# Performance work log

Hardware: AMD Instinct MI355X
Metric: run time of the kernel (lower is better)

The kernel has to match this reference:

```python
import jax, jax.numpy as jnp
import numpy as np
import math

B, S = 4, 1024
D_MODEL = 512
N_HEADS = 8
D_HEAD = D_MODEL // N_HEADS
D_FF = 2048
D_K_NEIGHBOR = 512.0
EPS_NORM = 1e-5
GN_EPS = 1e-5
LAMBDA_INIT = 0.8 - 0.6 * math.exp(-0.3 * 0.0)  # layer_idx = 0 -> 0.2


def _rmsnorm(x, w, eps=EPS_NORM):
    return x * jax.lax.rsqrt(jnp.mean(x * x, axis=-1, keepdims=True) + eps) * w


def _group_norm(x, gamma, beta):
    # x: [B, S, D]; torch GroupNorm(n_heads, d_model) applied on [B, D, S]:
    # normalize each (batch, group) over (d_head * S) elements, per-channel affine.
    b, s, d = x.shape
    xg = x.transpose(0, 2, 1).reshape(b, N_HEADS, D_HEAD, s)
    mean = xg.mean(axis=(2, 3), keepdims=True)
    var = ((xg - mean) ** 2).mean(axis=(2, 3), keepdims=True)
    xn = ((xg - mean) * jax.lax.rsqrt(var + GN_EPS)).reshape(b, d, s)
    xn = xn * gamma[None, :, None] + beta[None, :, None]
    return xn.transpose(0, 2, 1)


def setup_inputs() -> dict:
    key = jax.random.key(0)
    ks = jax.random.split(key, 20)
    sd = 1.0 / math.sqrt(D_MODEL)
    sdf = 1.0 / math.sqrt(D_FF)
    f32 = jnp.float32
    return {
        'x': jax.random.normal(ks[0], (B, S, D_MODEL), f32),
        'src_padding_mask': jax.random.randint(ks[1], (B, S), 0, 2).astype(jnp.int32),
        'learned_lambda': jnp.asarray(LAMBDA_INIT, f32),
        'wq_w': (jax.random.normal(ks[2], (D_MODEL, 2 * D_MODEL), f32) * sd),
        'wq_b': jnp.zeros((2 * D_MODEL,), f32),
        'wk_w': (jax.random.normal(ks[3], (D_MODEL, 2 * D_MODEL), f32) * sd),
        'wk_b': jnp.zeros((2 * D_MODEL,), f32),
        'wv_w': (jax.random.normal(ks[4], (D_MODEL, D_MODEL), f32) * sd),
        'wv_b': jnp.zeros((D_MODEL,), f32),
        'out_w': (jax.random.normal(ks[5], (D_MODEL, D_MODEL), f32) * sd),
        'out_b': jnp.zeros((D_MODEL,), f32),
        'gn_gamma': jnp.ones((D_MODEL,), f32),
        'gn_beta': jnp.zeros((D_MODEL,), f32),
        'aq_w': (jax.random.normal(ks[6], (D_MODEL, D_MODEL), f32) * sd),
        'aq_b': jnp.zeros((D_MODEL,), f32),
        'ak_w': (jax.random.normal(ks[7], (D_MODEL, D_MODEL), f32) * sd),
        'ak_b': jnp.zeros((D_MODEL,), f32),
        'wg_w': (jax.random.normal(ks[8], (D_MODEL, D_FF), f32) * sd),
        'w1_w': (jax.random.normal(ks[9], (D_MODEL, D_FF), f32) * sd),
        'w2_w': (jax.random.normal(ks[10], (D_FF, D_MODEL), f32) * sdf),
        'norm1_w': jnp.ones((D_MODEL,), f32),
        'norm2_w': jnp.ones((D_MODEL,), f32),
    }


def reference(x, src_padding_mask, learned_lambda,
              wq_w, wq_b, wk_w, wk_b, wv_w, wv_b, out_w, out_b,
              gn_gamma, gn_beta, aq_w, aq_b, ak_w, ak_b,
              wg_w, w1_w, w2_w, norm1_w, norm2_w):
    b, s, d = x.shape
    x_norm = _rmsnorm(x, norm1_w)

    # ---- neighbor affinity (layer_idx = 0 -> a = a_hat) ----
    Q = x_norm @ aq_w + aq_b
    K = x_norm @ ak_w + ak_b
    s_fwd = jnp.sum(Q[:, :-1] * K[:, 1:], axis=-1) / D_K_NEIGHBOR   # [B, S-1]
    s_bwd = jnp.sum(Q[:, 1:] * K[:, :-1], axis=-1) / D_K_NEIGHBOR
    a = 0.5 * (jax.nn.sigmoid(s_fwd) + jax.nn.sigmoid(s_bwd))        # [B, S-1]

    # ---- hierarchical mask: C[i,j] = prod(a[i:j]) = exp(L[j]-L[i]), symmetric ----
    # L is non-increasing (a in (0,1)), so prod(a[i:j]) = exp(-|L[i]-L[j]|); diag = 1.
    L = jnp.concatenate([jnp.zeros((b, 1), x.dtype), jnp.cumsum(jnp.log(a), axis=1)], axis=1)  # [B, S]
    C = jnp.exp(-jnp.abs(L[:, :, None] - L[:, None, :]))[:, None]   # [B,1,S,S]

    # ---- differential multi-head attention ----
    qp = x_norm @ wq_w + wq_b   # [B,S,2D]
    kp = x_norm @ wk_w + wk_b
    heads = lambda t: t.reshape(b, s, N_HEADS, D_HEAD).transpose(0, 2, 1, 3)
    q1, q2 = heads(qp[..., :D_MODEL]), heads(qp[..., D_MODEL:])
    k1, k2 = heads(kp[..., :D_MODEL]), heads(kp[..., D_MODEL:])
    v = heads(x_norm @ wv_w + wv_b)
    scale = 1.0 / math.sqrt(D_HEAD)
    sc1 = jnp.einsum('bhqd,bhkd->bhqk', q1, k1) * scale
    sc2 = jnp.einsum('bhqd,bhkd->bhqk', q2, k2) * scale
    pad = (src_padding_mask == 0)[:, None, None, :]
    sc1 = jnp.where(pad, -1e9, sc1)
    sc2 = jnp.where(pad, -1e9, sc2)
    aw1 = jax.nn.softmax(sc1, axis=-1)
    aw2 = jax.nn.softmax(sc2, axis=-1)
    comb = C * (aw1 - learned_lambda * aw2)
    ctx = jnp.einsum('bhqk,bhkd->bhqd', comb, v)
    ctx = ctx.transpose(0, 2, 1, 3).reshape(b, s, D_MODEL)
    ctx = _group_norm(ctx, gn_gamma, gn_beta) * (1.0 - LAMBDA_INIT)
    attn_out = ctx @ out_w + out_b

    # ---- residual + SwiGLU FFN (dropout = identity in eval) ----
    h = x + attn_out
    hn = _rmsnorm(h, norm2_w)
    ffn = (jax.nn.silu(hn @ wg_w) * (hn @ w1_w)) @ w2_w
    return h + ffn
```

## Files before the change

kernel.cpp:

```cpp
#include <hip/hip_runtime.h>
#include <math.h>

#define Bn 4
#define Sn 1024
#define DM 512
#define NH 8
#define DFF 2048
#define QKVN 2560

typedef __attribute__((ext_vector_type(8))) __bf16 bf16x8;
typedef __attribute__((ext_vector_type(2))) __bf16 bf16x2;
typedef __attribute__((ext_vector_type(4))) float f32x4;

#define MB (1u<<20)

__device__ __forceinline__ void gl_lds16(const void* g, void* l) {
    __builtin_amdgcn_global_load_lds(
        (const __attribute__((address_space(1))) void*)g,
        (__attribute__((address_space(3))) void*)l, 16, 0, 0);
}

struct TransBatch { const float* src[4]; __bf16* dst[4]; };

__global__ __launch_bounds__(256)
void transpose_kernel(TransBatch tb, int K, int N) {
    const float* w = tb.src[blockIdx.z];
    __bf16* wT = tb.dst[blockIdx.z];
    __shared__ float tile[32][33];
    int n0 = blockIdx.x * 32, k0 = blockIdx.y * 32;
    int tx = threadIdx.x, ty = threadIdx.y;
#pragma unroll
    for (int i = 0; i < 4; ++i)
        tile[ty + 8 * i][tx] = w[(size_t)(k0 + ty + 8 * i) * N + n0 + tx];
    __syncthreads();
#pragma unroll
    for (int i = 0; i < 4; ++i)
        wT[(size_t)(n0 + ty + 8 * i) * K + k0 + tx] = (__bf16)tile[tx][ty + 8 * i];
}

__global__ __launch_bounds__(256)
void pack_biases(const float* aq_b, const float* ak_b, const float* wq_b,
                 const float* wk_b, const float* wv_b,
                 float* aqk_b, float* qkv_b) {
    int t = blockIdx.x * 256 + threadIdx.x;
    if (t < 512) aqk_b[t] = aq_b[t];
    else if (t < 1024) aqk_b[t] = ak_b[t - 512];
    else if (t < 2048) qkv_b[t - 1024] = wq_b[t - 1024];
    else if (t < 3072) qkv_b[1024 + t - 2048] = wk_b[t - 2048];
    else if (t < 3584) qkv_b[2048 + t - 3072] = wv_b[t - 3072];
}

__global__ __launch_bounds__(256)
void rmsnorm_kernel(const float* __restrict__ x, const float* __restrict__ w,
                    __bf16* __restrict__ out) {
    int row = blockIdx.x;
    const float* xr = x + (size_t)row * DM;
    int t = threadIdx.x;
    float2 v = *(const float2*)&xr[2 * t];
    float ss = v.x * v.x + v.y * v.y;
#pragma unroll
    for (int off = 32; off; off >>= 1) ss += __shfl_xor(ss, off);
    __shared__ float red[4];
    int wid = t >> 6;
    if ((t & 63) == 0) red[wid] = ss;
    __syncthreads();
    float tot = red[0] + red[1] + red[2] + red[3];
    float rinv = rsqrtf(tot / (float)DM + 1e-5f);
    bf16x2 o;
    o[0] = (__bf16)(v.x * rinv * w[2 * t]);
    o[1] = (__bf16)(v.y * rinv * w[2 * t + 1]);
    *(bf16x2*)&out[(size_t)row * DM + 2 * t] = o;
}

template<int BM, int EPI>
__global__ __launch_bounds__(256)
void gemm_bf16(const __bf16* __restrict__ A, const __bf16* __restrict__ BT,
               const float* __restrict__ bias, const float* __restrict__ res,
               void* __restrict__ out, int M, int N, int K) {
    __shared__ __align__(16) char AsB[BM * 64];
    __shared__ __align__(16) char BsB[128 * 64];
    const int t = threadIdx.x;
    const int w = t >> 6, l = t & 63, c = l & 15, g = l >> 4;
    const int wr = w >> 1, wc = w & 1;
    const int bm = blockIdx.y * BM, bn = blockIdx.x * 128;
    constexpr int HM = BM / 2, WM = BM / 32;
    f32x4 acc[WM][4];
#pragma unroll
    for (int m = 0; m < WM; ++m)
#pragma unroll
        for (int n = 0; n < 4; ++n) acc[m][n] = (f32x4){0.f, 0.f, 0.f, 0.f};
    const int srow = t >> 2;
    const int kcol = ((t & 3) ^ ((t >> 3) & 3)) << 3;
    const __bf16* Ap = A + (size_t)(bm + srow) * K + kcol;
    const __bf16* Bp = BT + (size_t)(bn + srow) * K + kcol;
    char* dA = AsB + t * 16;
    char* dB = BsB + t * 16;
    char* dB2 = BsB + 4096 + t * 16;
    const int sw = (g ^ ((c >> 1) & 3)) << 4;
    for (int k0 = 0; k0 < K; k0 += 32) {
        gl_lds16(Ap + k0, dA);
        if constexpr (BM == 128) gl_lds16(Ap + (size_t)64 * K + k0, AsB + 4096 + t * 16);
        gl_lds16(Bp + k0, dB);
        gl_lds16(Bp + (size_t)64 * K + k0, dB2);
        __syncthreads();
        bf16x8 af[WM], bf_[4];
#pragma unroll
        for (int m = 0; m < WM; ++m)
            af[m] = *(const bf16x8*)(AsB + (wr * HM + m * 16 + c) * 64 + sw);
#pragma unroll
        for (int n = 0; n < 4; ++n)
            bf_[n] = *(const bf16x8*)(BsB + (wc * 64 + n * 16 + c) * 64 + sw);
#pragma unroll
        for (int m = 0; m < WM; ++m)
#pragma unroll
            for (int n = 0; n < 4; ++n)
                acc[m][n] = __builtin_amdgcn_mfma_f32_16x16x32_bf16(af[m], bf_[n], acc[m][n], 0, 0, 0);
        __syncthreads();
    }
#pragma unroll
    for (int m = 0; m < WM; ++m)
#pragma unroll
        for (int n = 0; n < 4; ++n) {
            int rowb = bm + wr * HM + m * 16 + 4 * g;
            int col = bn + wc * 64 + n * 16 + c;
            float bv = bias ? bias[col] : 0.f;
#pragma unroll
            for (int r = 0; r < 4; ++r) {
                size_t idx = (size_t)(rowb + r) * N + col;
                float val = acc[m][n][r] + bv;
                if constexpr (EPI == 0) {
                    ((__bf16*)out)[idx] = (__bf16)val;
                } else {
                    if (res) val += res[idx];
                    ((float*)out)[idx] = val;
                }
            }
        }
}

__global__ __launch_bounds__(256)
void gemm_swiglu(const __bf16* __restrict__ A, const __bf16* __restrict__ GT,
                 const __bf16* __restrict__ UT, __bf16* __restrict__ out,
                 int M, int N, int K) {
    __shared__ __align__(16) char AsB[128 * 64];
    __shared__ __align__(16) char GsB[128 * 64];
    __shared__ __align__(16) char UsB[128 * 64];
    const int t = threadIdx.x;
    const int w = t >> 6, l = t & 63, c = l & 15, g = l >> 4;
    const int wr = w >> 1, wc = w & 1;
    const int bm = blockIdx.y * 128, bn = blockIdx.x * 128;
    f32x4 accg[4][4], accu[4][4];
#pragma unroll
    for (int m = 0; m < 4; ++m)
#pragma unroll
        for (int n = 0; n < 4; ++n) {
            accg[m][n] = (f32x4){0.f, 0.f, 0.f, 0.f};
            accu[m][n] = (f32x4){0.f, 0.f, 0.f, 0.f};
        }
    const int srow = t >> 2;
    const int kcol = ((t & 3) ^ ((t >> 3) & 3)) << 3;
    const __bf16* Ap = A + (size_t)(bm + srow) * K + kcol;
    const __bf16* Gp = GT + (size_t)(bn + srow) * K + kcol;
    const __bf16* Up = UT + (size_t)(bn + srow) * K + kcol;
    const int sw = (g ^ ((c >> 1) & 3)) << 4;
    for (int k0 = 0; k0 < K; k0 += 32) {
        gl_lds16(Ap + k0, AsB + t * 16);
        gl_lds16(Ap + (size_t)64 * K + k0, AsB + 4096 + t * 16);
        gl_lds16(Gp + k0, GsB + t * 16);
        gl_lds16(Gp + (size_t)64 * K + k0, GsB + 4096 + t * 16);
        gl_lds16(Up + k0, UsB + t * 16);
        gl_lds16(Up + (size_t)64 * K + k0, UsB + 4096 + t * 16);
        __syncthreads();
        bf16x8 af[4], gf[4], uf[4];
#pragma unroll
        for (int m = 0; m < 4; ++m)
            af[m] = *(const bf16x8*)(AsB + (wr * 64 + m * 16 + c) * 64 + sw);
#pragma unroll
        for (int n = 0; n < 4; ++n) {
            gf[n] = *(const bf16x8*)(GsB + (wc * 64 + n * 16 + c) * 64 + sw);
            uf[n] = *(const bf16x8*)(UsB + (wc * 64 + n * 16 + c) * 64 + sw);
        }
#pragma unroll
        for (int m = 0; m < 4; ++m)
#pragma unroll
            for (int n = 0; n < 4; ++n) {
                accg[m][n] = __builtin_amdgcn_mfma_f32_16x16x32_bf16(af[m], gf[n], accg[m][n], 0, 0, 0);
                accu[m][n] = __builtin_amdgcn_mfma_f32_16x16x32_bf16(af[m], uf[n], accu[m][n], 0, 0, 0);
            }
        __syncthreads();
    }
#pragma unroll
    for (int m = 0; m < 4; ++m)
#pragma unroll
        for (int n = 0; n < 4; ++n) {
            int rowb = bm + wr * 64 + m * 16 + 4 * g;
            int col = bn + wc * 64 + n * 16 + c;
#pragma unroll
            for (int r = 0; r < 4; ++r) {
                float gv = accg[m][n][r];
                float uv = accu[m][n][r];
                float sg = gv / (1.f + __expf(-gv));
                out[(size_t)(rowb + r) * N + col] = (__bf16)(sg * uv);
            }
        }
}

__global__ __launch_bounds__(256)
void affinity_dots(const __bf16* __restrict__ aqk, float* __restrict__ la) {
    int i = blockIdx.x * 256 + threadIdx.x;
    int b = blockIdx.y;
    if (i >= Sn - 1) { la[b * Sn + i] = 0.f; return; }
    const __bf16* Qi = aqk + (size_t)(b * Sn + i) * 1024;
    const __bf16* Ki = Qi + 512;
    float sf = 0.f, sb = 0.f;
#pragma unroll 4
    for (int d = 0; d < DM / 8; ++d) {
        bf16x8 q0 = *(const bf16x8*)(Qi + d * 8);
        bf16x8 q1 = *(const bf16x8*)(Qi + 1024 + d * 8);
        bf16x8 k0 = *(const bf16x8*)(Ki + d * 8);
        bf16x8 k1 = *(const bf16x8*)(Ki + 1024 + d * 8);
#pragma unroll
        for (int j = 0; j < 8; ++j) {
            sf += (float)q0[j] * (float)k1[j];
            sb += (float)q1[j] * (float)k0[j];
        }
    }
    sf *= (1.f / 512.f);
    sb *= (1.f / 512.f);
    float a = 0.5f * (1.f / (1.f + __expf(-sf)) + 1.f / (1.f + __expf(-sb)));
    la[b * Sn + i] = __logf(a);
}

__global__ __launch_bounds__(256)
void scan_kernel(const float* __restrict__ la, float* __restrict__ L) {
    int b = blockIdx.x, j = threadIdx.x;
    __shared__ float sc[256];
    float4 v = *(const float4*)&la[b * Sn + 4 * j];
    float s0 = v.x, s1 = s0 + v.y, s2 = s1 + v.z, s3 = s2 + v.w;
    sc[j] = s3;
    __syncthreads();
    for (int off = 1; off < 256; off <<= 1) {
        float add = (j >= off) ? sc[j - off] : 0.f;
        __syncthreads();
        sc[j] += add;
        __syncthreads();
    }
    float base = sc[j] - s3;
    if (j == 0) L[b * Sn] = 0.f;
    L[b * Sn + 4 * j + 1] = base + s0;
    L[b * Sn + 4 * j + 2] = base + s1;
    L[b * Sn + 4 * j + 3] = base + s2;
    if (4 * j + 4 < Sn) L[b * Sn + 4 * j + 4] = base + s3;
}

__global__ __launch_bounds__(256)
void attn_mfma(const __bf16* __restrict__ qkv, const float* __restrict__ L,
               const int* __restrict__ mask, const float* __restrict__ lam_p,
               float* __restrict__ ctx) {
    int x = blockIdx.x;
    int xcd = x & 7, idx = x >> 3;
    int bh = xcd * 4 + (idx >> 4);
    int qb = idx & 15;
    int b = bh >> 3, h = bh & 7;
    const int t = threadIdx.x;
    const int w = t >> 6, l = t & 63, c = l & 15, g = l >> 4;

    __shared__ __align__(16) char KldsB[64 * 256];
    __shared__ __align__(16) char VtB[64 * 128];
    __shared__ __align__(16) char PldsB[2][64 * 128];
    __shared__ float Lk_s[64];
    __shared__ float msk_s[64];
    __shared__ float fs_s[2][64];
    __shared__ float ls_s[2][64];

    const int q0 = qb * 64;
    const int qg = q0 + 16 * w + c;
    float Lq = L[b * Sn + qg];
    float lam = lam_p[0];
    bf16x8 qf[2][2];
#pragma unroll
    for (int mat = 0; mat < 2; ++mat)
#pragma unroll
        for (int dh = 0; dh < 2; ++dh)
            qf[mat][dh] = *(const bf16x8*)(qkv + (size_t)(b * Sn + qg) * QKVN + mat * 512 + h * 64 + dh * 32 + g * 8);
    f32x4 O[2][4];
#pragma unroll
    for (int mat = 0; mat < 2; ++mat)
#pragma unroll
        for (int nd = 0; nd < 4; ++nd) O[mat][nd] = (f32x4){0.f, 0.f, 0.f, 0.f};
    float m_run[2] = {-INFINITY, -INFINITY};
    float l_run[2] = {0.f, 0.f};
    const int cs = c & 7;

    for (int kt = 0; kt < 16; ++kt) {
        const size_t kbase = (size_t)(b * Sn + kt * 64);
#pragma unroll
        for (int rep = 0; rep < 4; ++rep) {
            int krow = rep * 16 + (t >> 4);
            int mat = (t >> 3) & 1;
            int lg = (t & 7) ^ (krow & 7);
            gl_lds16(qkv + (kbase + krow) * QKVN + 1024 + mat * 512 + h * 64 + lg * 8,
                     KldsB + rep * 4096 + t * 16);
        }
#pragma unroll
        for (int rep = 0; rep < 2; ++rep) {
            int k = l;
            int dg = rep * 4 + w;
            bf16x8 val = *(const bf16x8*)(qkv + (kbase + k) * QKVN + 2048 + h * 64 + dg * 8);
#pragma unroll
            for (int j = 0; j < 8; ++j)
                *(__bf16*)(VtB + (dg * 8 + j) * 128 + ((((k >> 3) ^ j) << 4) | ((k & 7) << 1))) = val[j];
        }
        if (t < 64) {
            Lk_s[t] = L[b * Sn + kt * 64 + t];
            msk_s[t] = (float)mask[b * Sn + kt * 64 + t];
        }
        __syncthreads();
        float Cv[16], msel[16];
#pragma unroll
        for (int kf = 0; kf < 4; ++kf)
#pragma unroll
            for (int r = 0; r < 4; ++r) {
                int kk = kf * 16 + 4 * g + r;
                Cv[kf * 4 + r] = __expf(-fabsf(Lq - Lk_s[kk]));
                msel[kf * 4 + r] = msk_s[kk];
            }
#pragma unroll
        for (int mat = 0; mat < 2; ++mat) {
            f32x4 s[4];
            __builtin_amdgcn_s_setprio(1);
#pragma unroll
            for (int kf = 0; kf < 4; ++kf) {
                f32x4 a = (f32x4){0.f, 0.f, 0.f, 0.f};
#pragma unroll
                for (int dh = 0; dh < 2; ++dh) {
                    bf16x8 kfr = *(const bf16x8*)(KldsB + (kf * 16 + c) * 256 + (mat * 8 + ((dh * 4 + g) ^ cs)) * 16);
                    a = __builtin_amdgcn_mfma_f32_16x16x32_bf16(kfr, qf[mat][dh], a, 0, 0, 0);
                }
                s[kf] = a;
            }
            __builtin_amdgcn_s_setprio(0);
            float tm = -INFINITY;
#pragma unroll
            for (int kf = 0; kf < 4; ++kf)
#pragma unroll
                for (int r = 0; r < 4; ++r) {
                    float sv = (msel[kf * 4 + r] != 0.f) ? s[kf][r] * 0.125f : -1e9f;
                    s[kf][r] = sv;
                    tm = fmaxf(tm, sv);
                }
            tm = fmaxf(tm, __shfl_xor(tm, 16));
            tm = fmaxf(tm, __shfl_xor(tm, 32));
            float mn = fmaxf(m_run[mat], tm);
            float f = __expf(m_run[mat] - mn);
            m_run[mat] = mn;
            if (g == 0) fs_s[mat][16 * w + c] = f;
            float es = 0.f;
#pragma unroll
            for (int kf = 0; kf < 4; ++kf) {
                bf16x2 p01, p23;
                float e0 = __expf(s[kf][0] - mn);
                float e1 = __expf(s[kf][1] - mn);
                float e2 = __expf(s[kf][2] - mn);
                float e3 = __expf(s[kf][3] - mn);
                es += (e0 + e1) + (e2 + e3);
                p01[0] = (__bf16)(e0 * Cv[kf * 4 + 0]);
                p01[1] = (__bf16)(e1 * Cv[kf * 4 + 1]);
                p23[0] = (__bf16)(e2 * Cv[kf * 4 + 2]);
                p23[1] = (__bf16)(e3 * Cv[kf * 4 + 3]);
                char* pb = PldsB[mat] + (16 * w + c) * 128 + (((kf * 2 + (g >> 1)) ^ cs) << 4) + ((g & 1) << 3);
                *(bf16x2*)pb = p01;
                *(bf16x2*)(pb + 4) = p23;
            }
            es += __shfl_xor(es, 16);
            es += __shfl_xor(es, 32);
            l_run[mat] = l_run[mat] * f + es;
        }
        __syncthreads();
#pragma unroll
        for (int mat = 0; mat < 2; ++mat) {
            f32x4 fv = *(const f32x4*)&fs_s[mat][16 * w + 4 * g];
#pragma unroll
            for (int nd = 0; nd < 4; ++nd) O[mat][nd] *= fv;
            __builtin_amdgcn_s_setprio(1);
#pragma unroll
            for (int kh = 0; kh < 2; ++kh) {
                bf16x8 pa = *(const bf16x8*)(PldsB[mat] + (16 * w + c) * 128 + (((kh * 4 + g) ^ cs) << 4));
#pragma unroll
                for (int nd = 0; nd < 4; ++nd) {
                    bf16x8 vb = *(const bf16x8*)(VtB + (nd * 16 + c) * 128 + (((kh * 4 + g) ^ cs) << 4));
                    O[mat][nd] = __builtin_amdgcn_mfma_f32_16x16x32_bf16(pa, vb, O[mat][nd], 0, 0, 0);
                }
            }
            __builtin_amdgcn_s_setprio(0);
        }
        __syncthreads();
    }
    if (g == 0) {
        ls_s[0][16 * w + c] = l_run[0];
        ls_s[1][16 * w + c] = l_run[1];
    }
    __syncthreads();
    f32x4 l1 = *(const f32x4*)&ls_s[0][16 * w + 4 * g];
    f32x4 l2 = *(const f32x4*)&ls_s[1][16 * w + 4 * g];
#pragma unroll
    for (int nd = 0; nd < 4; ++nd)
#pragma unroll
        for (int r = 0; r < 4; ++r) {
            float val = O[0][nd][r] / l1[r] - lam * (O[1][nd][r] / l2[r]);
            int q = q0 + 16 * w + 4 * g + r;
            ctx[(size_t)(b * Sn + q) * DM + h * 64 + nd * 16 + c] = val;
        }
}

__global__ __launch_bounds__(256)
void gn_stats(const float* __restrict__ ctx, float* __restrict__ stats) {
    int b = blockIdx.x >> 3, h = blockIdx.x & 7;
    int s0 = blockIdx.y * 128;
    int t = threadIdx.x;
    float sum = 0.f, sq = 0.f;
    for (int i = t; i < 128 * 32; i += 256) {
        int s = s0 + (i >> 5), dp = (i & 31) * 2;
        float2 vv = *(const float2*)&ctx[(size_t)(b * Sn + s) * DM + h * 64 + dp];
        sum += vv.x + vv.y;
        sq += vv.x * vv.x + vv.y * vv.y;
    }
#pragma unroll
    for (int off = 32; off; off >>= 1) {
        sum += __shfl_xor(sum, off);
        sq += __shfl_xor(sq, off);
    }
    __shared__ float rs[4], rq[4];
    int wid = t >> 6;
    if ((t & 63) == 0) { rs[wid] = sum; rq[wid] = sq; }
    __syncthreads();
    if (t == 0) {
        atomicAdd(&stats[blockIdx.x * 2], rs[0] + rs[1] + rs[2] + rs[3]);
        atomicAdd(&stats[blockIdx.x * 2 + 1], rq[0] + rq[1] + rq[2] + rq[3]);
    }
}

__global__ __launch_bounds__(256)
void gn_apply(const float* __restrict__ ctx, const float* __restrict__ stats,
              const float* __restrict__ gamma, const float* __restrict__ beta,
              __bf16* __restrict__ out) {
    int row = blockIdx.x;
    int b = row >> 10;
    int t = threadIdx.x;
    int dpair = t * 2;
    int h = dpair >> 6;
    float mean = stats[(b * 8 + h) * 2] * (1.f / 65536.f);
    float msq = stats[(b * 8 + h) * 2 + 1] * (1.f / 65536.f);
    float rinv = rsqrtf(msq - mean * mean + 1e-5f);
    size_t off_ = (size_t)row * DM + dpair;
    float2 vv = *(const float2*)&ctx[off_];
    bf16x2 o;
    o[0] = (__bf16)(((vv.x - mean) * rinv * gamma[dpair] + beta[dpair]) * 0.8f);
    o[1] = (__bf16)(((vv.y - mean) * rinv * gamma[dpair + 1] + beta[dpair + 1]) * 0.8f);
    *(bf16x2*)&out[off_] = o;
}

extern "C" void kernel_launch(void* const* d_in, const int* in_sizes, int n_in,
                              void* d_out, int out_size, void* d_ws, size_t ws_size,
                              hipStream_t stream) {
    const float* x        = (const float*)d_in[0];
    const int*   mask     = (const int*)d_in[1];
    const float* lam      = (const float*)d_in[2];
    const float* wq_w     = (const float*)d_in[3];
    const float* wq_b     = (const float*)d_in[4];
    const float* wk_w     = (const float*)d_in[5];
    const float* wk_b     = (const float*)d_in[6];
    const float* wv_w     = (const float*)d_in[7];
    const float* wv_b     = (const float*)d_in[8];
    const float* out_w    = (const float*)d_in[9];
    const float* out_b    = (const float*)d_in[10];
    const float* gn_gamma = (const float*)d_in[11];
    const float* gn_beta  = (const float*)d_in[12];
    const float* aq_w     = (const float*)d_in[13];
    const float* aq_b     = (const float*)d_in[14];
    const float* ak_w     = (const float*)d_in[15];
    const float* ak_b     = (const float*)d_in[16];
    const float* wg_w     = (const float*)d_in[17];
    const float* w1_w     = (const float*)d_in[18];
    const float* w2_w     = (const float*)d_in[19];
    const float* norm1_w  = (const float*)d_in[20];
    const float* norm2_w  = (const float*)d_in[21];

    char* ws = (char*)d_ws;
    __bf16* aqkT = (__bf16*)(ws + 0);
    __bf16* qkvT = (__bf16*)(ws + 1 * MB);
    __bf16* outT = (__bf16*)(ws + 7 * MB / 2);
    __bf16* wgT  = (__bf16*)(ws + 4 * MB);
    __bf16* w1T  = (__bf16*)(ws + 6 * MB);
    __bf16* w2T  = (__bf16*)(ws + 8 * MB);
    __bf16* xn   = (__bf16*)(ws + 10 * MB);
    __bf16* aqk  = (__bf16*)(ws + 14 * MB);
    __bf16* qkv  = (__bf16*)(ws + 22 * MB);
    float*  la   = (float*)(ws + 42 * MB);
    float*  Lb   = (float*)(ws + 42 * MB + 64 * 1024);
    float*  stats= (float*)(ws + 42 * MB + 128 * 1024);
    float*  aqk_b= (float*)(ws + 42 * MB + 192 * 1024);
    float*  qkv_b= (float*)(ws + 42 * MB + 256 * 1024);
    float*  ctx  = (float*)(ws + 43 * MB);
    __bf16* ctxb = (__bf16*)(ws + 51 * MB);
    float*  h    = (float*)(ws + 55 * MB);
    __bf16* hn   = (__bf16*)(ws + 14 * MB);
    __bf16* mid  = (__bf16*)(ws + 22 * MB);
    float*  outp = (float*)d_out;

    const int M = Bn * Sn;
    dim3 thr(32, 8);

    hipMemsetAsync(stats, 0, 64 * sizeof(float), stream);

    TransBatch ta = {{aq_w, ak_w, wv_w, out_w},
                     {aqkT, aqkT + 512 * 512, qkvT + (size_t)2048 * 512, outT}};
    transpose_kernel<<<dim3(16, 16, 4), thr, 0, stream>>>(ta, 512, 512);
    TransBatch tbq = {{wq_w, wk_w, nullptr, nullptr},
                      {qkvT, qkvT + (size_t)1024 * 512, nullptr, nullptr}};
    transpose_kernel<<<dim3(32, 16, 2), thr, 0, stream>>>(tbq, 512, 1024);
    TransBatch tc = {{wg_w, w1_w, nullptr, nullptr}, {wgT, w1T, nullptr, nullptr}};
    transpose_kernel<<<dim3(64, 16, 2), thr, 0, stream>>>(tc, 512, 2048);
    TransBatch td = {{w2_w, nullptr, nullptr, nullptr}, {w2T, nullptr, nullptr, nullptr}};
    transpose_kernel<<<dim3(16, 64, 1), thr, 0, stream>>>(td, 2048, 512);

    pack_biases<<<14, 256, 0, stream>>>(aq_b, ak_b, wq_b, wk_b, wv_b, aqk_b, qkv_b);

    rmsnorm_kernel<<<M, 256, 0, stream>>>(x, norm1_w, xn);

    gemm_bf16<64, 0><<<dim3(8, 64), 256, 0, stream>>>(xn, aqkT, aqk_b, nullptr, aqk, M, 1024, 512);
    affinity_dots<<<dim3(4, 4), 256, 0, stream>>>(aqk, la);
    scan_kernel<<<Bn, 256, 0, stream>>>(la, Lb);

    gemm_bf16<128, 0><<<dim3(20, 32), 256, 0, stream>>>(xn, qkvT, qkv_b, nullptr, qkv, M, QKVN, 512);

    attn_mfma<<<512, 256, 0, stream>>>(qkv, Lb, mask, lam, ctx);

    gn_stats<<<dim3(32, 8), 256, 0, stream>>>(ctx, stats);
    gn_apply<<<M, 256, 0, stream>>>(ctx, stats, gn_gamma, gn_beta, ctxb);

    gemm_bf16<64, 1><<<dim3(4, 64), 256, 0, stream>>>(ctxb, outT, out_b, x, h, M, 512, 512);

    rmsnorm_kernel<<<M, 256, 0, stream>>>(h, norm2_w, hn);

    gemm_swiglu<<<dim3(16, 32), 256, 0, stream>>>(hn, wgT, w1T, mid, M, DFF, 512);

    gemm_bf16<64, 1><<<dim3(4, 64), 256, 0, stream>>>(mid, w2T, nullptr, h, outp, M, 512, DFF);
}
```

Before: 366.1 us.

## Split differential attention streams across 8 waves and shrink N tile for D=512 GEMMs

```diff
diff --git a/kernel.cpp b/kernel.cpp
--- a/kernel.cpp
+++ b/kernel.cpp
@@ -72,57 +72,54 @@
     *(bf16x2*)&out[(size_t)row * DM + 2 * t] = o;
 }
 
-template<int BM, int EPI>
+template<int BM, int BN, int EPI>
 __global__ __launch_bounds__(256)
 void gemm_bf16(const __bf16* __restrict__ A, const __bf16* __restrict__ BT,
                const float* __restrict__ bias, const float* __restrict__ res,
                void* __restrict__ out, int M, int N, int K) {
     __shared__ __align__(16) char AsB[BM * 64];
-    __shared__ __align__(16) char BsB[128 * 64];
+    __shared__ __align__(16) char BsB[BN * 64];
     const int t = threadIdx.x;
     const int w = t >> 6, l = t & 63, c = l & 15, g = l >> 4;
     const int wr = w >> 1, wc = w & 1;
-    const int bm = blockIdx.y * BM, bn = blockIdx.x * 128;
-    constexpr int HM = BM / 2, WM = BM / 32;
-    f32x4 acc[WM][4];
+    const int bm = blockIdx.y * BM, bn = blockIdx.x * BN;
+    constexpr int HM = BM / 2, WM = BM / 32, HN = BN / 2, WN = BN / 32;
+    f32x4 acc[WM][WN];
 #pragma unroll
     for (int m = 0; m < WM; ++m)
 #pragma unroll
-        for (int n = 0; n < 4; ++n) acc[m][n] = (f32x4){0.f, 0.f, 0.f, 0.f};
+        for (int n = 0; n < WN; ++n) acc[m][n] = (f32x4){0.f, 0.f, 0.f, 0.f};
     const int srow = t >> 2;
     const int kcol = ((t & 3) ^ ((t >> 3) & 3)) << 3;
     const __bf16* Ap = A + (size_t)(bm + srow) * K + kcol;
     const __bf16* Bp = BT + (size_t)(bn + srow) * K + kcol;
-    char* dA = AsB + t * 16;
-    char* dB = BsB + t * 16;
-    char* dB2 = BsB + 4096 + t * 16;
     const int sw = (g ^ ((c >> 1) & 3)) << 4;
     for (int k0 = 0; k0 < K; k0 += 32) {
-        gl_lds16(Ap + k0, dA);
+        gl_lds16(Ap + k0, AsB + t * 16);
         if constexpr (BM == 128) gl_lds16(Ap + (size_t)64 * K + k0, AsB + 4096 + t * 16);
-        gl_lds16(Bp + k0, dB);
-        gl_lds16(Bp + (size_t)64 * K + k0, dB2);
-        __syncthreads();
-        bf16x8 af[WM], bf_[4];
+        gl_lds16(Bp + k0, BsB + t * 16);
+        if constexpr (BN == 128) gl_lds16(Bp + (size_t)64 * K + k0, BsB + 4096 + t * 16);
+        __syncthreads();
+        bf16x8 af[WM], bf_[WN];
 #pragma unroll
         for (int m = 0; m < WM; ++m)
             af[m] = *(const bf16x8*)(AsB + (wr * HM + m * 16 + c) * 64 + sw);
 #pragma unroll
-        for (int n = 0; n < 4; ++n)
-            bf_[n] = *(const bf16x8*)(BsB + (wc * 64 + n * 16 + c) * 64 + sw);
+        for (int n = 0; n < WN; ++n)
+            bf_[n] = *(const bf16x8*)(BsB + (wc * HN + n * 16 + c) * 64 + sw);
 #pragma unroll
         for (int m = 0; m < WM; ++m)
 #pragma unroll
-            for (int n = 0; n < 4; ++n)
+            for (int n = 0; n < WN; ++n)
                 acc[m][n] = __builtin_amdgcn_mfma_f32_16x16x32_bf16(af[m], bf_[n], acc[m][n], 0, 0, 0);
         __syncthreads();
     }
 #pragma unroll
     for (int m = 0; m < WM; ++m)
 #pragma unroll
-        for (int n = 0; n < 4; ++n) {
+        for (int n = 0; n < WN; ++n) {
             int rowb = bm + wr * HM + m * 16 + 4 * g;
-            int col = bn + wc * 64 + n * 16 + c;
+            int col = bn + wc * HN + n * 16 + c;
             float bv = bias ? bias[col] : 0.f;
 #pragma unroll
             for (int r = 0; r < 4; ++r) {
@@ -253,7 +250,7 @@
     if (4 * j + 4 < Sn) L[b * Sn + 4 * j + 4] = base + s3;
 }
 
-__global__ __launch_bounds__(256)
+__global__ __launch_bounds__(512)
 void attn_mfma(const __bf16* __restrict__ qkv, const float* __restrict__ L,
                const int* __restrict__ mask, const float* __restrict__ lam_p,
                float* __restrict__ ctx) {
@@ -264,6 +261,7 @@
     int b = bh >> 3, h = bh & 7;
     const int t = threadIdx.x;
     const int w = t >> 6, l = t & 63, c = l & 15, g = l >> 4;
+    const int mat = w >> 2, ws = w & 3;
 
     __shared__ __align__(16) char KldsB[64 * 256];
     __shared__ __align__(16) char VtB[64 * 128];
@@ -274,38 +272,34 @@
     __shared__ float ls_s[2][64];
 
     const int q0 = qb * 64;
-    const int qg = q0 + 16 * w + c;
+    const int qg = q0 + 16 * ws + c;
     float Lq = L[b * Sn + qg];
     float lam = lam_p[0];
-    bf16x8 qf[2][2];
-#pragma unroll
-    for (int mat = 0; mat < 2; ++mat)
-#pragma unroll
-        for (int dh = 0; dh < 2; ++dh)
-            qf[mat][dh] = *(const bf16x8*)(qkv + (size_t)(b * Sn + qg) * QKVN + mat * 512 + h * 64 + dh * 32 + g * 8);
-    f32x4 O[2][4];
-#pragma unroll
-    for (int mat = 0; mat < 2; ++mat)
-#pragma unroll
-        for (int nd = 0; nd < 4; ++nd) O[mat][nd] = (f32x4){0.f, 0.f, 0.f, 0.f};
-    float m_run[2] = {-INFINITY, -INFINITY};
-    float l_run[2] = {0.f, 0.f};
+    bf16x8 qf[2];
+#pragma unroll
+    for (int dh = 0; dh < 2; ++dh)
+        qf[dh] = *(const bf16x8*)(qkv + (size_t)(b * Sn + qg) * QKVN + mat * 512 + h * 64 + dh * 32 + g * 8);
+    f32x4 O[4];
+#pragma unroll
+    for (int nd = 0; nd < 4; ++nd) O[nd] = (f32x4){0.f, 0.f, 0.f, 0.f};
+    float m_run = -INFINITY;
+    float l_run = 0.f;
     const int cs = c & 7;
 
     for (int kt = 0; kt < 16; ++kt) {
         const size_t kbase = (size_t)(b * Sn + kt * 64);
 #pragma unroll
-        for (int rep = 0; rep < 4; ++rep) {
-            int krow = rep * 16 + (t >> 4);
-            int mat = (t >> 3) & 1;
-            int lg = (t & 7) ^ (krow & 7);
-            gl_lds16(qkv + (kbase + krow) * QKVN + 1024 + mat * 512 + h * 64 + lg * 8,
-                     KldsB + rep * 4096 + t * 16);
-        }
-#pragma unroll
         for (int rep = 0; rep < 2; ++rep) {
-            int k = l;
-            int dg = rep * 4 + w;
+            int u = t & 255;
+            int rr = (t >> 8) + 2 * rep;
+            int krow = rr * 16 + (u >> 4);
+            int km = (u >> 3) & 1;
+            int lg = (u & 7) ^ (krow & 7);
+            gl_lds16(qkv + (kbase + krow) * QKVN + 1024 + km * 512 + h * 64 + lg * 8,
+                     KldsB + rr * 4096 + u * 16);
+        }
+        {
+            int k = t & 63, dg = t >> 6;
             bf16x8 val = *(const bf16x8*)(qkv + (kbase + k) * QKVN + 2048 + h * 64 + dg * 8);
 #pragma unroll
             for (int j = 0; j < 8; ++j)
@@ -316,101 +310,107 @@
             msk_s[t] = (float)mask[b * Sn + kt * 64 + t];
         }
         __syncthreads();
-        float Cv[16], msel[16];
+        float Cv[16];
+        unsigned mbits = 0;
 #pragma unroll
         for (int kf = 0; kf < 4; ++kf)
 #pragma unroll
             for (int r = 0; r < 4; ++r) {
                 int kk = kf * 16 + 4 * g + r;
                 Cv[kf * 4 + r] = __expf(-fabsf(Lq - Lk_s[kk]));
-                msel[kf * 4 + r] = msk_s[kk];
-            }
-#pragma unroll
-        for (int mat = 0; mat < 2; ++mat) {
-            f32x4 s[4];
-            __builtin_amdgcn_s_setprio(1);
-#pragma unroll
-            for (int kf = 0; kf < 4; ++kf) {
-                f32x4 a = (f32x4){0.f, 0.f, 0.f, 0.f};
-#pragma unroll
-                for (int dh = 0; dh < 2; ++dh) {
-                    bf16x8 kfr = *(const bf16x8*)(KldsB + (kf * 16 + c) * 256 + (mat * 8 + ((dh * 4 + g) ^ cs)) * 16);
-                    a = __builtin_amdgcn_mfma_f32_16x16x32_bf16(kfr, qf[mat][dh], a, 0, 0, 0);
-                }
-                s[kf] = a;
-            }
-            __builtin_amdgcn_s_setprio(0);
-            float tm = -INFINITY;
-#pragma unroll
-            for (int kf = 0; kf < 4; ++kf)
-#pragma unroll
-                for (int r = 0; r < 4; ++r) {
-                    float sv = (msel[kf * 4 + r] != 0.f) ? s[kf][r] * 0.125f : -1e9f;
-                    s[kf][r] = sv;
-                    tm = fmaxf(tm, sv);
-                }
-            tm = fmaxf(tm, __shfl_xor(tm, 16));
-            tm = fmaxf(tm, __shfl_xor(tm, 32));
-            float mn = fmaxf(m_run[mat], tm);
-            float f = __expf(m_run[mat] - mn);
-            m_run[mat] = mn;
-            if (g == 0) fs_s[mat][16 * w + c] = f;
-            float es = 0.f;
-#pragma unroll
-            for (int kf = 0; kf < 4; ++kf) {
-                bf16x2 p01, p23;
-                float e0 = __expf(s[kf][0] - mn);
-                float e1 = __expf(s[kf][1] - mn);
-                float e2 = __expf(s[kf][2] - mn);
-                float e3 = __expf(s[kf][3] - mn);
-                es += (e0 + e1) + (e2 + e3);
-                p01[0] = (__bf16)(e0 * Cv[kf * 4 + 0]);
-                p01[1] = (__bf16)(e1 * Cv[kf * 4 + 1]);
-                p23[0] = (__bf16)(e2 * Cv[kf * 4 + 2]);
-                p23[1] = (__bf16)(e3 * Cv[kf * 4 + 3]);
-                char* pb = PldsB[mat] + (16 * w + c) * 128 + (((kf * 2 + (g >> 1)) ^ cs) << 4) + ((g & 1) << 3);
-                *(bf16x2*)pb = p01;
-                *(bf16x2*)(pb + 4) = p23;
-            }
-            es += __shfl_xor(es, 16);
-            es += __shfl_xor(es, 32);
-            l_run[mat] = l_run[mat] * f + es;
-        }
-        __syncthreads();
-#pragma unroll
-        for (int mat = 0; mat < 2; ++mat) {
-            f32x4 fv = *(const f32x4*)&fs_s[mat][16 * w + 4 * g];
-#pragma unroll
-            for (int nd = 0; nd < 4; ++nd) O[mat][nd] *= fv;
-            __builtin_amdgcn_s_setprio(1);
-#pragma unroll
-            for (int kh = 0; kh < 2; ++kh) {
-                bf16x8 pa = *(const bf16x8*)(PldsB[mat] + (16 * w + c) * 128 + (((kh * 4 + g) ^ cs) << 4));
-#pragma unroll
-                for (int nd = 0; nd < 4; ++nd) {
-                    bf16x8 vb = *(const bf16x8*)(VtB + (nd * 16 + c) * 128 + (((kh * 4 + g) ^ cs) << 4));
-                    O[mat][nd] = __builtin_amdgcn_mfma_f32_16x16x32_bf16(pa, vb, O[mat][nd], 0, 0, 0);
-                }
-            }
-            __builtin_amdgcn_s_setprio(0);
-        }
-        __syncthreads();
-    }
-    if (g == 0) {
-        ls_s[0][16 * w + c] = l_run[0];
-        ls_s[1][16 * w + c] = l_run[1];
-    }
+                mbits |= (msk_s[kk] != 0.f ? 1u : 0u) << (kf * 4 + r);
+            }
+        f32x4 s[4];
+        __builtin_amdgcn_s_setprio(1);
+#pragma unroll
+        for (int kf = 0; kf < 4; ++kf) {
+            f32x4 a = (f32x4){0.f, 0.f, 0.f, 0.f};
+#pragma unroll
+            for (int dh = 0; dh < 2; ++dh) {
+                bf16x8 kfr = *(const bf16x8*)(KldsB + (kf * 16 + c) * 256 + (mat * 8 + ((dh * 4 + g) ^ cs)) * 16);
+                a = __builtin_amdgcn_mfma_f32_16x16x32_bf16(kfr, qf[dh], a, 0, 0, 0);
+            }
+            s[kf] = a;
+        }
+        __builtin_amdgcn_s_setprio(0);
+        float tm = -INFINITY;
+#pragma unroll
+        for (int kf = 0; kf < 4; ++kf)
+#pragma unroll
+            for (int r = 0; r < 4; ++r) {
+                float sv = ((mbits >> (kf * 4 + r)) & 1u) ? s[kf][r] * 0.125f : -1e9f;
+                s[kf][r] = sv;
+                tm = fmaxf(tm, sv);
+            }
+        tm = fmaxf(tm, __shfl_xor(tm, 16));
+        tm = fmaxf(tm, __shfl_xor(tm, 32));
+        float mn = fmaxf(m_run, tm);
+        float f = __expf(m_run - mn);
+        m_run = mn;
+        if (g == 0) fs_s[mat][16 * ws + c] = f;
+        float es = 0.f;
+#pragma unroll
+        for (int kf = 0; kf < 4; ++kf) {
+            bf16x2 p01, p23;
+            float e0 = __expf(s[kf][0] - mn);
+            float e1 = __expf(s[kf][1] - mn);
+            float e2 = __expf(s[kf][2] - mn);
+            float e3 = __expf(s[kf][3] - mn);
+            es += (e0 + e1) + (e2 + e3);
+            p01[0] = (__bf16)(e0 * Cv[kf * 4 + 0]);
+            p01[1] = (__bf16)(e1 * Cv[kf * 4 + 1]);
+            p23[0] = (__bf16)(e2 * Cv[kf * 4 + 2]);
+            p23[1] = (__bf16)(e3 * Cv[kf * 4 + 3]);
+            char* pb = PldsB[mat] + (16 * ws + c) * 128 + (((kf * 2 + (g >> 1)) ^ cs) << 4) + ((g & 1) << 3);
+            *(bf16x2*)pb = p01;
+            *(bf16x2*)(pb + 4) = p23;
+        }
+        es += __shfl_xor(es, 16);
+        es += __shfl_xor(es, 32);
+        l_run = l_run * f + es;
+        __syncthreads();
+        f32x4 fv = *(const f32x4*)&fs_s[mat][16 * ws + 4 * g];
+#pragma unroll
+        for (int nd = 0; nd < 4; ++nd) O[nd] *= fv;
+        __builtin_amdgcn_s_setprio(1);
+#pragma unroll
+        for (int kh = 0; kh < 2; ++kh) {
+            bf16x8 pa = *(const bf16x8*)(PldsB[mat] + (16 * ws + c) * 128 + (((kh * 4 + g) ^ cs) << 4));
+#pragma unroll
+            for (int nd = 0; nd < 4; ++nd) {
+                bf16x8 vb = *(const bf16x8*)(VtB + (nd * 16 + c) * 128 + (((kh * 4 + g) ^ cs) << 4));
+                O[nd] = __builtin_amdgcn_mfma_f32_16x16x32_bf16(pa, vb, O[nd], 0, 0, 0);
+            }
+        }
+        __builtin_amdgcn_s_setprio(0);
+        __syncthreads();
+    }
+    if (g == 0) ls_s[mat][16 * ws + c] = l_run;
     __syncthreads();
-    f32x4 l1 = *(const f32x4*)&ls_s[0][16 * w + 4 * g];
-    f32x4 l2 = *(const f32x4*)&ls_s[1][16 * w + 4 * g];
+    f32x4 lv = *(const f32x4*)&ls_s[mat][16 * ws + 4 * g];
 #pragma unroll
     for (int nd = 0; nd < 4; ++nd)
 #pragma unroll
-        for (int r = 0; r < 4; ++r) {
-            float val = O[0][nd][r] / l1[r] - lam * (O[1][nd][r] / l2[r]);
-            int q = q0 + 16 * w + 4 * g + r;
-            ctx[(size_t)(b * Sn + q) * DM + h * 64 + nd * 16 + c] = val;
-        }
+        for (int r = 0; r < 4; ++r) O[nd][r] /= lv[r];
+    float* Pf = (float*)PldsB;
+    if (mat == 1) {
+#pragma unroll
+        for (int nd = 0; nd < 4; ++nd)
+#pragma unroll
+            for (int r = 0; r < 4; ++r)
+                Pf[(16 * ws + 4 * g + r) * 64 + nd * 16 + c] = O[nd][r];
+    }
+    __syncthreads();
+    if (mat == 0) {
+#pragma unroll
+        for (int nd = 0; nd < 4; ++nd)
+#pragma unroll
+            for (int r = 0; r < 4; ++r) {
+                float val = O[nd][r] - lam * Pf[(16 * ws + 4 * g + r) * 64 + nd * 16 + c];
+                int q = q0 + 16 * ws + 4 * g + r;
+                ctx[(size_t)(b * Sn + q) * DM + h * 64 + nd * 16 + c] = val;
+            }
+    }
 }
 
 __global__ __launch_bounds__(256)
@@ -528,22 +528,22 @@
 
     rmsnorm_kernel<<<M, 256, 0, stream>>>(x, norm1_w, xn);
 
-    gemm_bf16<64, 0><<<dim3(8, 64), 256, 0, stream>>>(xn, aqkT, aqk_b, nullptr, aqk, M, 1024, 512);
+    gemm_bf16<64, 128, 0><<<dim3(8, 64), 256, 0, stream>>>(xn, aqkT, aqk_b, nullptr, aqk, M, 1024, 512);
     affinity_dots<<<dim3(4, 4), 256, 0, stream>>>(aqk, la);
     scan_kernel<<<Bn, 256, 0, stream>>>(la, Lb);
 
-    gemm_bf16<128, 0><<<dim3(20, 32), 256, 0, stream>>>(xn, qkvT, qkv_b, nullptr, qkv, M, QKVN, 512);
-
-    attn_mfma<<<512, 256, 0, stream>>>(qkv, Lb, mask, lam, ctx);
+    gemm_bf16<128, 128, 0><<<dim3(20, 32), 256, 0, stream>>>(xn, qkvT, qkv_b, nullptr, qkv, M, QKVN, 512);
+
+    attn_mfma<<<512, 512, 0, stream>>>(qkv, Lb, mask, lam, ctx);
 
     gn_stats<<<dim3(32, 8), 256, 0, stream>>>(ctx, stats);
     gn_apply<<<M, 256, 0, stream>>>(ctx, stats, gn_gamma, gn_beta, ctxb);
 
-    gemm_bf16<64, 1><<<dim3(4, 64), 256, 0, stream>>>(ctxb, outT, out_b, x, h, M, 512, 512);
+    gemm_bf16<64, 64, 1><<<dim3(8, 64), 256, 0, stream>>>(ctxb, outT, out_b, x, h, M, 512, 512);
 
     rmsnorm_kernel<<<M, 256, 0, stream>>>(h, norm2_w, hn);
 
     gemm_swiglu<<<dim3(16, 32), 256, 0, stream>>>(hn, wgT, w1T, mid, M, DFF, 512);
 
-    gemm_bf16<64, 1><<<dim3(4, 64), 256, 0, stream>>>(mid, w2T, nullptr, h, outp, M, 512, DFF);
-}
+    gemm_bf16<64, 64, 1><<<dim3(8, 64), 256, 0, stream>>>(mid, w2T, nullptr, h, outp, M, 512, DFF);
+}
```

After: 352.1 us. 1.04x faster.
